# Performance work log

Hardware: AMD Instinct MI355X
Metric: run time of the kernel (lower is better)

The kernel has to match this reference:

```python
import jax, jax.numpy as jnp
import numpy as np

N_NODES = 50000
N_EDGES = 600000
N_GRAPHS = 500
HID = 128
N_LAYERS = 3
N_CLASSES = 10


def setup_inputs() -> dict:
    key = jax.random.key(0)
    ks = jax.random.split(key, 10)
    x = jax.random.normal(ks[0], (N_NODES, HID), dtype=jnp.float32)
    edge_attr = jax.random.normal(ks[1], (N_EDGES, 4), dtype=jnp.float32)
    edge_index = jax.random.randint(ks[2], (2, N_EDGES), 0, N_NODES, dtype=jnp.int32)
    batch = jnp.sort(jax.random.randint(ks[3], (N_NODES,), 0, N_GRAPHS, dtype=jnp.int32))
    s = 1.0 / np.sqrt(HID)
    Wl = jax.random.normal(ks[4], (N_LAYERS, HID, HID), dtype=jnp.float32) * s
    bl = jax.random.normal(ks[5], (N_LAYERS, HID), dtype=jnp.float32) * s
    Wr = jax.random.normal(ks[6], (N_LAYERS, HID, HID), dtype=jnp.float32) * s
    W1 = jax.random.normal(ks[7], (HID, HID), dtype=jnp.float32) * s
    b1 = jnp.zeros((HID,), dtype=jnp.float32)
    W2 = jax.random.normal(ks[8], (N_CLASSES, HID), dtype=jnp.float32) * s
    b2 = jnp.zeros((N_CLASSES,), dtype=jnp.float32)
    return {"x": x, "edge_attr": edge_attr, "edge_index": edge_index, "batch": batch,
            "Wl": Wl, "bl": bl, "Wr": Wr, "W1": W1, "b1": b1, "W2": W2, "b2": b2}


def _sage_conv(x, src, dst, Wl_i, bl_i, Wr_i):
    # mean aggregation of source-node features at target nodes (PyG SAGEConv)
    msg_sum = jax.ops.segment_sum(x[src], dst, num_segments=N_NODES)  # [N, H]
    cnt = jax.ops.segment_sum(jnp.ones((src.shape[0],), x.dtype), dst, num_segments=N_NODES)
    mean = msg_sum / jnp.maximum(cnt, 1.0)[:, None]
    return mean @ Wl_i.T + bl_i + x @ Wr_i.T


def reference(x, edge_attr, edge_index, batch, Wl, bl, Wr, W1, b1, W2, b2):
    # edge_attr is ignored by SAGEConv
    src, dst = edge_index[0], edge_index[1]
    for i in range(N_LAYERS):
        x = jax.nn.relu(_sage_conv(x, src, dst, Wl[i], bl[i], Wr[i]))
    # global_add_pool over graphs
    g = jax.ops.segment_sum(x, batch, num_segments=N_GRAPHS)  # [G, H]
    g = jax.nn.relu(g)
    # dropout p=0.5 is identity at inference
    h = jax.nn.relu(g @ W1.T + b1)
    logits = h @ W2.T + b2
    return jax.nn.log_softmax(logits, axis=1)
```

## Files before the change

kernel.cpp:

```cpp
#include <hip/hip_runtime.h>
#include <math.h>

#define HID 128
#define NCLS 10
#define MAXDEG 32
#define TROWS 32
#define MSP 136

typedef __attribute__((ext_vector_type(8))) short frag8;
typedef __attribute__((ext_vector_type(8))) unsigned short u16x8;
typedef __attribute__((ext_vector_type(4))) float f32x4;

static __device__ __forceinline__ float relu_f(float v) { return v > 0.f ? v : 0.f; }

static __device__ __forceinline__ unsigned short f2bf(float f) {
    unsigned int u = __float_as_uint(f);
    u += 0x7fffu + ((u >> 16) & 1u);
    return (unsigned short)(u >> 16);
}
static __device__ __forceinline__ float bf2f(unsigned short u) {
    return __uint_as_float(((unsigned int)u) << 16);
}

static __device__ __forceinline__ void conv4(const float* __restrict__ in,
                                             unsigned short* __restrict__ out, int i) {
    float4 v = *(const float4*)&in[i * 4];
    ushort4 o;
    o.x = f2bf(v.x); o.y = f2bf(v.y); o.z = f2bf(v.z); o.w = f2bf(v.w);
    *(ushort4*)&out[i * 4] = o;
}

__global__ __launch_bounds__(256) void prep_kernel(const float* __restrict__ x, unsigned short* __restrict__ xb, int nx4,
                                                   const float* __restrict__ Wl, unsigned short* __restrict__ wlb, int nwl4,
                                                   const float* __restrict__ Wr, unsigned short* __restrict__ wrb, int nwr4,
                                                   int* __restrict__ deg, int ndeg4) {
    int i = blockIdx.x * blockDim.x + threadIdx.x;
    if (i < nx4) { conv4(x, xb, i); return; }
    i -= nx4;
    if (i < nwl4) { conv4(Wl, wlb, i); return; }
    i -= nwl4;
    if (i < nwr4) { conv4(Wr, wrb, i); return; }
    i -= nwr4;
    if (i < ndeg4) *(int4*)&deg[i * 4] = make_int4(0, 0, 0, 0);
}

__global__ void fill_kernel(const int* __restrict__ src, const int* __restrict__ dst,
                            int* __restrict__ deg, unsigned short* __restrict__ col, int nE) {
    int e = blockIdx.x * blockDim.x + threadIdx.x;
    if (e < nE) {
        int d = dst[e];
        int p = atomicAdd(&deg[d], 1);
        if (p < MAXDEG) col[(long)d * MAXDEG + p] = (unsigned short)src[e];
    }
}

__global__ __launch_bounds__(256, 6) void sage_kernel(const unsigned short* __restrict__ Xb,
                                                      const int* __restrict__ deg,
                                                      const unsigned short* __restrict__ col,
                                                      const unsigned short* __restrict__ Wlb,
                                                      const unsigned short* __restrict__ Wrb,
                                                      const float* __restrict__ bl,
                                                      unsigned short* __restrict__ Yb, int nN) {
    __shared__ unsigned short ms[TROWS * MSP];

    const int r0 = blockIdx.x * TROWS;

    {
        const int grp = threadIdx.x >> 4;
        const int l16 = threadIdx.x & 15;
        const long fo = (long)l16 * 8;
        for (int i = 0; i < 2; ++i) {
            const int nl = grp * 2 + i;
            const int n = r0 + nl;
            const int d = (n < nN) ? min(deg[n], MAXDEG) : 0;
            const unsigned short* cp = col + (long)n * MAXDEG;

            float acc[8] = {0, 0, 0, 0, 0, 0, 0, 0};

            int p = 0;
            for (; p + 8 <= d; p += 8) {
                int s0 = cp[p],     s1 = cp[p + 1], s2 = cp[p + 2], s3 = cp[p + 3];
                int s4 = cp[p + 4], s5 = cp[p + 5], s6 = cp[p + 6], s7 = cp[p + 7];
                u16x8 v0 = *(const u16x8*)&Xb[(long)s0 * HID + fo];
                u16x8 v1 = *(const u16x8*)&Xb[(long)s1 * HID + fo];
                u16x8 v2 = *(const u16x8*)&Xb[(long)s2 * HID + fo];
                u16x8 v3 = *(const u16x8*)&Xb[(long)s3 * HID + fo];
                u16x8 v4 = *(const u16x8*)&Xb[(long)s4 * HID + fo];
                u16x8 v5 = *(const u16x8*)&Xb[(long)s5 * HID + fo];
                u16x8 v6 = *(const u16x8*)&Xb[(long)s6 * HID + fo];
                u16x8 v7 = *(const u16x8*)&Xb[(long)s7 * HID + fo];
#pragma unroll
                for (int j = 0; j < 8; ++j)
                    acc[j] += ((bf2f(v0[j]) + bf2f(v1[j])) + (bf2f(v2[j]) + bf2f(v3[j]))) +
                              ((bf2f(v4[j]) + bf2f(v5[j])) + (bf2f(v6[j]) + bf2f(v7[j])));
            }
            if (p + 4 <= d) {
                int s0 = cp[p], s1 = cp[p + 1], s2 = cp[p + 2], s3 = cp[p + 3];
                u16x8 v0 = *(const u16x8*)&Xb[(long)s0 * HID + fo];
                u16x8 v1 = *(const u16x8*)&Xb[(long)s1 * HID + fo];
                u16x8 v2 = *(const u16x8*)&Xb[(long)s2 * HID + fo];
                u16x8 v3 = *(const u16x8*)&Xb[(long)s3 * HID + fo];
#pragma unroll
                for (int j = 0; j < 8; ++j)
                    acc[j] += (bf2f(v0[j]) + bf2f(v1[j])) + (bf2f(v2[j]) + bf2f(v3[j]));
                p += 4;
            }
            if (p < d) {
                int s0 = cp[p];
                int s1 = cp[min(p + 1, MAXDEG - 1)];
                int s2 = cp[min(p + 2, MAXDEG - 1)];
                int s3 = cp[min(p + 3, MAXDEG - 1)];
                u16x8 v0 = *(const u16x8*)&Xb[(long)s0 * HID + fo];
                u16x8 v1 = *(const u16x8*)&Xb[(long)s1 * HID + fo];
                u16x8 v2 = *(const u16x8*)&Xb[(long)s2 * HID + fo];
                u16x8 v3 = *(const u16x8*)&Xb[(long)s3 * HID + fo];
#pragma unroll
                for (int j = 0; j < 8; ++j) acc[j] += bf2f(v0[j]);
                if (p + 1 < d) {
#pragma unroll
                    for (int j = 0; j < 8; ++j) acc[j] += bf2f(v1[j]);
                }
                if (p + 2 < d) {
#pragma unroll
                    for (int j = 0; j < 8; ++j) acc[j] += bf2f(v2[j]);
                }
                if (p + 3 < d) {
#pragma unroll
                    for (int j = 0; j < 8; ++j) acc[j] += bf2f(v3[j]);
                }
            }

            const float inv = 1.f / fmaxf((float)d, 1.f);
            u16x8 o;
#pragma unroll
            for (int j = 0; j < 8; ++j) o[j] = f2bf(acc[j] * inv);
            *(u16x8*)&ms[nl * MSP + l16 * 8] = o;
        }
    }
    __syncthreads();

    const int lane = threadIdx.x & 63;
    const int wave = threadIdx.x >> 6;
    const int l15 = lane & 15;
    const int quad = lane >> 4;
    const int wr = wave & 1;
    const int wc = wave >> 1;

    f32x4 acc[4];
#pragma unroll
    for (int ct = 0; ct < 4; ++ct) acc[ct] = (f32x4){0.f, 0.f, 0.f, 0.f};

#pragma unroll
    for (int ks = 0; ks < HID; ks += 32) {
        const int lrow = wr * 16 + l15;
        frag8 aM = *(const frag8*)&ms[lrow * MSP + ks + quad * 8];
        frag8 aX = *(const frag8*)&Xb[(long)(r0 + lrow) * HID + ks + quad * 8];
#pragma unroll
        for (int ct = 0; ct < 4; ++ct) {
            const long nrow = wc * 64 + ct * 16 + l15;
            frag8 bL = *(const frag8*)&Wlb[nrow * HID + ks + quad * 8];
            frag8 bR = *(const frag8*)&Wrb[nrow * HID + ks + quad * 8];
            acc[ct] = __builtin_amdgcn_mfma_f32_16x16x32_bf16(aM, bL, acc[ct], 0, 0, 0);
            acc[ct] = __builtin_amdgcn_mfma_f32_16x16x32_bf16(aX, bR, acc[ct], 0, 0, 0);
        }
    }

#pragma unroll
    for (int ct = 0; ct < 4; ++ct) {
        const int gc = wc * 64 + ct * 16 + l15;
        const float bb = bl[gc];
#pragma unroll
        for (int reg = 0; reg < 4; ++reg) {
            const int gm = r0 + wr * 16 + quad * 4 + reg;
            if (gm < nN) {
                const float v = relu_f(acc[ct][reg] + bb);
                Yb[(long)gm * HID + gc] = f2bf(v);
            }
        }
    }
}

__global__ __launch_bounds__(128) void poolmlp_kernel(const unsigned short* __restrict__ xb,
                                                      const int* __restrict__ batch, int nN,
                                                      const float* __restrict__ W1,
                                                      const float* __restrict__ b1,
                                                      const float* __restrict__ W2,
                                                      const float* __restrict__ b2,
                                                      float* __restrict__ out) {
    __shared__ float gs[HID];
    __shared__ float hs[HID];
    __shared__ float ls[NCLS];
    __shared__ float red[2];
    int gid = blockIdx.x;
    int j = threadIdx.x;

    int lo = 0, hi = nN;
    while (lo < hi) { int mid = (lo + hi) >> 1; if (batch[mid] < gid) lo = mid + 1; else hi = mid; }
    int s = lo;
    hi = nN;
    while (lo < hi) { int mid = (lo + hi) >> 1; if (batch[mid] < gid + 1) lo = mid + 1; else hi = mid; }
    int e = lo;

    float a0 = 0.f, a1 = 0.f, a2 = 0.f, a3 = 0.f;
    int n = s;
    for (; n + 4 <= e; n += 4) {
        a0 += bf2f(xb[(long)n * HID + j]);
        a1 += bf2f(xb[(long)(n + 1) * HID + j]);
        a2 += bf2f(xb[(long)(n + 2) * HID + j]);
        a3 += bf2f(xb[(long)(n + 3) * HID + j]);
    }
    for (; n < e; ++n) a0 += bf2f(xb[(long)n * HID + j]);
    gs[j] = relu_f((a0 + a1) + (a2 + a3));
    __syncthreads();

    float acc = b1[j];
#pragma unroll 8
    for (int k = 0; k < HID; ++k) acc += gs[k] * W1[j * HID + k];
    hs[j] = relu_f(acc);
    __syncthreads();
    if (j < NCLS) {
        float lg = b2[j];
#pragma unroll 8
        for (int k = 0; k < HID; ++k) lg += hs[k] * W2[j * HID + k];
        ls[j] = lg;
    }
    __syncthreads();
    if (j == 0) {
        float m = ls[0];
        for (int c = 1; c < NCLS; ++c) m = fmaxf(m, ls[c]);
        float sum = 0.f;
        for (int c = 0; c < NCLS; ++c) sum += expf(ls[c] - m);
        red[0] = m;
        red[1] = logf(sum);
    }
    __syncthreads();
    if (j < NCLS) out[gid * NCLS + j] = ls[j] - red[0] - red[1];
}


extern "C" void kernel_launch(void* const* d_in, const int* in_sizes, int n_in,
                              void* d_out, int out_size, void* d_ws, size_t ws_size,
                              hipStream_t stream) {
    const float* x_in  = (const float*)d_in[0];
    const int*   eidx  = (const int*)d_in[2];
    const int*   batch = (const int*)d_in[3];
    const float* Wl    = (const float*)d_in[4];
    const float* bl    = (const float*)d_in[5];
    const float* Wr    = (const float*)d_in[6];
    const float* W1    = (const float*)d_in[7];
    const float* b1    = (const float*)d_in[8];
    const float* W2    = (const float*)d_in[9];
    const float* b2    = (const float*)d_in[10];
    float* out = (float*)d_out;

    const int nN = in_sizes[0] / HID;
    const int nE = in_sizes[2] / 2;
    const int nG = out_size / NCLS;
    const int nWl = in_sizes[4];
    const int nWr = in_sizes[6];
    const int nNp = (nN + TROWS - 1) & ~(TROWS - 1);
    const int nTiles = nNp / TROWS;

    const int* src = eidx;
    const int* dst = eidx + nE;

    char* p = (char*)d_ws;
    auto carve = [&](size_t bytes) {
        char* r = p;
        p += (bytes + 255) & ~(size_t)255;
        return r;
    };
    unsigned short* xb  = (unsigned short*)carve((size_t)nNp * HID * 2);
    unsigned short* yb0 = (unsigned short*)carve((size_t)nNp * HID * 2);
    unsigned short* yb1 = (unsigned short*)carve((size_t)nNp * HID * 2);
    unsigned short* wlb = (unsigned short*)carve((size_t)nWl * 2);
    unsigned short* wrb = (unsigned short*)carve((size_t)nWr * 2);
    int*   deg = (int*)carve((size_t)nN * 4);
    unsigned short* col = (unsigned short*)carve((size_t)nN * MAXDEG * 2);
    (void)ws_size; (void)n_in;

    const int nx4 = nN * HID / 4, nwl4 = nWl / 4, nwr4 = nWr / 4, ndeg4 = (nN + 3) / 4;
    const int prep_total = nx4 + nwl4 + nwr4 + ndeg4;
    prep_kernel<<<(prep_total + 255) / 256, 256, 0, stream>>>(
        x_in, xb, nx4, Wl, wlb, nwl4, Wr, wrb, nwr4, deg, ndeg4);

    fill_kernel<<<(nE + 255) / 256, 256, 0, stream>>>(src, dst, deg, col, nE);

    const unsigned short* xcur = xb;
    unsigned short* bufs[2] = {yb0, yb1};
    for (int l = 0; l < 3; ++l) {
        sage_kernel<<<nTiles, 256, 0, stream>>>(
            xcur, deg, col,
            wlb + (size_t)l * HID * HID, wrb + (size_t)l * HID * HID,
            bl + (size_t)l * HID, bufs[l & 1], nN);
        xcur = bufs[l & 1];
    }

    poolmlp_kernel<<<nG, 128, 0, stream>>>(xcur, batch, nN, W1, b1, W2, b2, out);
}
```

Baseline: 316.3 us.

## Stage neighbor gathers via direct global-to-LDS loads with zero-row padding

Replaces the per-thread register gather of neighbor features with global_load_lds (direct global-to-LDS DMA) into per-wave staging buffers, issuing 8 loads per chunk and consuming them with staggered vmcnt waits. Column lists are prefilled with a dummy index pointing at zeroed padding rows, so unused slots gather zeros and tail branches disappear. Neighbor indices are broadcast with shuffles. This adds 32 KB of LDS per block and lowers the launch-bounds occupancy hint from 6 to 3. It also loads full chunks of 8 even for low-degree nodes, which wastes bandwidth, and inline waitcnt asm is fragile.

```diff
diff --git a/kernel.cpp b/kernel.cpp
--- a/kernel.cpp
+++ b/kernel.cpp
@@ -20,6 +20,12 @@
 }
 static __device__ __forceinline__ float bf2f(unsigned short u) {
     return __uint_as_float(((unsigned int)u) << 16);
+}
+
+static __device__ __forceinline__ void gld_lds16(const void* g, void* l) {
+    __builtin_amdgcn_global_load_lds((const __attribute__((address_space(1))) unsigned int*)g,
+                                     (__attribute__((address_space(3))) unsigned int*)l,
+                                     16, 0, 0);
 }
 
 static __device__ __forceinline__ void conv4(const float* __restrict__ in,
@@ -33,7 +39,10 @@
 __global__ __launch_bounds__(256) void prep_kernel(const float* __restrict__ x, unsigned short* __restrict__ xb, int nx4,
                                                    const float* __restrict__ Wl, unsigned short* __restrict__ wlb, int nwl4,
                                                    const float* __restrict__ Wr, unsigned short* __restrict__ wrb, int nwr4,
-                                                   int* __restrict__ deg, int ndeg4) {
+                                                   int* __restrict__ deg, int ndeg4,
+                                                   uint4* __restrict__ colp, int ncol8, unsigned int zpat,
+                                                   uint4* __restrict__ zp0, uint4* __restrict__ zp1,
+                                                   uint4* __restrict__ zp2, int nz8) {
     int i = blockIdx.x * blockDim.x + threadIdx.x;
     if (i < nx4) { conv4(x, xb, i); return; }
     i -= nx4;
@@ -41,7 +50,15 @@
     i -= nwl4;
     if (i < nwr4) { conv4(Wr, wrb, i); return; }
     i -= nwr4;
-    if (i < ndeg4) *(int4*)&deg[i * 4] = make_int4(0, 0, 0, 0);
+    if (i < ndeg4) { *(int4*)&deg[i * 4] = make_int4(0, 0, 0, 0); return; }
+    i -= ndeg4;
+    if (i < ncol8) { colp[i] = make_uint4(zpat, zpat, zpat, zpat); return; }
+    i -= ncol8;
+    if (i < nz8) { zp0[i] = make_uint4(0, 0, 0, 0); return; }
+    i -= nz8;
+    if (i < nz8) { zp1[i] = make_uint4(0, 0, 0, 0); return; }
+    i -= nz8;
+    if (i < nz8) zp2[i] = make_uint4(0, 0, 0, 0);
 }
 
 __global__ void fill_kernel(const int* __restrict__ src, const int* __restrict__ dst,
@@ -54,7 +71,7 @@
     }
 }
 
-__global__ __launch_bounds__(256, 6) void sage_kernel(const unsigned short* __restrict__ Xb,
+__global__ __launch_bounds__(256, 3) void sage_kernel(const unsigned short* __restrict__ Xb,
                                                       const int* __restrict__ deg,
                                                       const unsigned short* __restrict__ col,
                                                       const unsigned short* __restrict__ Wlb,
@@ -62,85 +79,56 @@
                                                       const float* __restrict__ bl,
                                                       unsigned short* __restrict__ Yb, int nN) {
     __shared__ unsigned short ms[TROWS * MSP];
+    __shared__ unsigned short stg[4 * 4096];
 
     const int r0 = blockIdx.x * TROWS;
-
-    {
-        const int grp = threadIdx.x >> 4;
-        const int l16 = threadIdx.x & 15;
-        const long fo = (long)l16 * 8;
-        for (int i = 0; i < 2; ++i) {
-            const int nl = grp * 2 + i;
-            const int n = r0 + nl;
-            const int d = (n < nN) ? min(deg[n], MAXDEG) : 0;
-            const unsigned short* cp = col + (long)n * MAXDEG;
-
-            float acc[8] = {0, 0, 0, 0, 0, 0, 0, 0};
-
-            int p = 0;
-            for (; p + 8 <= d; p += 8) {
-                int s0 = cp[p],     s1 = cp[p + 1], s2 = cp[p + 2], s3 = cp[p + 3];
-                int s4 = cp[p + 4], s5 = cp[p + 5], s6 = cp[p + 6], s7 = cp[p + 7];
-                u16x8 v0 = *(const u16x8*)&Xb[(long)s0 * HID + fo];
-                u16x8 v1 = *(const u16x8*)&Xb[(long)s1 * HID + fo];
-                u16x8 v2 = *(const u16x8*)&Xb[(long)s2 * HID + fo];
-                u16x8 v3 = *(const u16x8*)&Xb[(long)s3 * HID + fo];
-                u16x8 v4 = *(const u16x8*)&Xb[(long)s4 * HID + fo];
-                u16x8 v5 = *(const u16x8*)&Xb[(long)s5 * HID + fo];
-                u16x8 v6 = *(const u16x8*)&Xb[(long)s6 * HID + fo];
-                u16x8 v7 = *(const u16x8*)&Xb[(long)s7 * HID + fo];
-#pragma unroll
-                for (int j = 0; j < 8; ++j)
-                    acc[j] += ((bf2f(v0[j]) + bf2f(v1[j])) + (bf2f(v2[j]) + bf2f(v3[j]))) +
-                              ((bf2f(v4[j]) + bf2f(v5[j])) + (bf2f(v6[j]) + bf2f(v7[j])));
-            }
-            if (p + 4 <= d) {
-                int s0 = cp[p], s1 = cp[p + 1], s2 = cp[p + 2], s3 = cp[p + 3];
-                u16x8 v0 = *(const u16x8*)&Xb[(long)s0 * HID + fo];
-                u16x8 v1 = *(const u16x8*)&Xb[(long)s1 * HID + fo];
-                u16x8 v2 = *(const u16x8*)&Xb[(long)s2 * HID + fo];
-                u16x8 v3 = *(const u16x8*)&Xb[(long)s3 * HID + fo];
-#pragma unroll
-                for (int j = 0; j < 8; ++j)
-                    acc[j] += (bf2f(v0[j]) + bf2f(v1[j])) + (bf2f(v2[j]) + bf2f(v3[j]));
-                p += 4;
-            }
-            if (p < d) {
-                int s0 = cp[p];
-                int s1 = cp[min(p + 1, MAXDEG - 1)];
-                int s2 = cp[min(p + 2, MAXDEG - 1)];
-                int s3 = cp[min(p + 3, MAXDEG - 1)];
-                u16x8 v0 = *(const u16x8*)&Xb[(long)s0 * HID + fo];
-                u16x8 v1 = *(const u16x8*)&Xb[(long)s1 * HID + fo];
-                u16x8 v2 = *(const u16x8*)&Xb[(long)s2 * HID + fo];
-                u16x8 v3 = *(const u16x8*)&Xb[(long)s3 * HID + fo];
-#pragma unroll
-                for (int j = 0; j < 8; ++j) acc[j] += bf2f(v0[j]);
-                if (p + 1 < d) {
-#pragma unroll
-                    for (int j = 0; j < 8; ++j) acc[j] += bf2f(v1[j]);
+    const int lane = threadIdx.x & 63;
+    const int wave = threadIdx.x >> 6;
+    const int grp4 = lane >> 4;
+    const int l16 = lane & 15;
+    const int fo = l16 * 8;
+    unsigned short* stg_w = &stg[wave * 4096];
+
+#pragma unroll
+    for (int set = 0; set < 2; ++set) {
+        const int nl = wave * 8 + set * 4 + grp4;
+        const int n = r0 + nl;
+        const int d = min(deg[n], MAXDEG);
+        const unsigned short* cp = col + (long)n * MAXDEG;
+        const int il = cp[l16];
+        const int ih = cp[16 + l16];
+
+        float acc[8] = {0, 0, 0, 0, 0, 0, 0, 0};
+
+#pragma unroll
+        for (int c = 0; c < 4; ++c) {
+            const bool act = (c * 8 < d);
+            if (act) {
+                asm volatile("s_waitcnt lgkmcnt(0)" ::: "memory");
+#pragma unroll
+                for (int k = 0; k < 8; ++k) {
+                    const int slot = c * 8 + k;
+                    const int idx = (slot < 16) ? __shfl(il, slot, 16) : __shfl(ih, slot - 16, 16);
+                    gld_lds16(Xb + (long)idx * HID + fo, stg_w + k * 512);
                 }
-                if (p + 2 < d) {
-#pragma unroll
-                    for (int j = 0; j < 8; ++j) acc[j] += bf2f(v2[j]);
-                }
-                if (p + 3 < d) {
-#pragma unroll
-                    for (int j = 0; j < 8; ++j) acc[j] += bf2f(v3[j]);
+#pragma unroll
+                for (int k = 0; k < 8; ++k) {
+                    asm volatile("s_waitcnt vmcnt(%0)" ::"i"(7 - k) : "memory");
+                    u16x8 v = *(const u16x8*)&stg_w[k * 512 + lane * 8];
+#pragma unroll
+                    for (int j = 0; j < 8; ++j) acc[j] += bf2f(v[j]);
                 }
             }
-
-            const float inv = 1.f / fmaxf((float)d, 1.f);
-            u16x8 o;
-#pragma unroll
-            for (int j = 0; j < 8; ++j) o[j] = f2bf(acc[j] * inv);
-            *(u16x8*)&ms[nl * MSP + l16 * 8] = o;
         }
-    }
-    __syncthreads();
-
-    const int lane = threadIdx.x & 63;
-    const int wave = threadIdx.x >> 6;
+
+        const float inv = 1.f / fmaxf((float)d, 1.f);
+        u16x8 o;
+#pragma unroll
+        for (int j = 0; j < 8; ++j) o[j] = f2bf(acc[j] * inv);
+        *(u16x8*)&ms[nl * MSP + fo] = o;
+    }
+    __syncthreads();
+
     const int l15 = lane & 15;
     const int quad = lane >> 4;
     const int wr = wave & 1;
@@ -260,6 +248,7 @@
     const int nWr = in_sizes[6];
     const int nNp = (nN + TROWS - 1) & ~(TROWS - 1);
     const int nTiles = nNp / TROWS;
+    const int nRows = nNp + 8;
 
     const int* src = eidx;
     const int* dst = eidx + nE;
@@ -270,19 +259,27 @@
         p += (bytes + 255) & ~(size_t)255;
         return r;
     };
-    unsigned short* xb  = (unsigned short*)carve((size_t)nNp * HID * 2);
-    unsigned short* yb0 = (unsigned short*)carve((size_t)nNp * HID * 2);
-    unsigned short* yb1 = (unsigned short*)carve((size_t)nNp * HID * 2);
+    unsigned short* xb  = (unsigned short*)carve((size_t)nRows * HID * 2);
+    unsigned short* yb0 = (unsigned short*)carve((size_t)nRows * HID * 2);
+    unsigned short* yb1 = (unsigned short*)carve((size_t)nRows * HID * 2);
     unsigned short* wlb = (unsigned short*)carve((size_t)nWl * 2);
     unsigned short* wrb = (unsigned short*)carve((size_t)nWr * 2);
-    int*   deg = (int*)carve((size_t)nN * 4);
-    unsigned short* col = (unsigned short*)carve((size_t)nN * MAXDEG * 2);
+    int*   deg = (int*)carve((size_t)nNp * 4);
+    unsigned short* col = (unsigned short*)carve((size_t)nNp * MAXDEG * 2);
     (void)ws_size; (void)n_in;
 
-    const int nx4 = nN * HID / 4, nwl4 = nWl / 4, nwr4 = nWr / 4, ndeg4 = (nN + 3) / 4;
-    const int prep_total = nx4 + nwl4 + nwr4 + ndeg4;
+    const int nx4 = nN * HID / 4, nwl4 = nWl / 4, nwr4 = nWr / 4;
+    const int ndeg4 = (nNp + 3) / 4;
+    const int ncol8 = nNp * MAXDEG / 8;
+    const int nzrows = nNp + 1 - nN;
+    const int nz8 = nzrows * HID / 8;
+    const unsigned int zpat = (unsigned int)nNp | ((unsigned int)nNp << 16);
+    const int prep_total = nx4 + nwl4 + nwr4 + ndeg4 + ncol8 + 3 * nz8;
     prep_kernel<<<(prep_total + 255) / 256, 256, 0, stream>>>(
-        x_in, xb, nx4, Wl, wlb, nwl4, Wr, wrb, nwr4, deg, ndeg4);
+        x_in, xb, nx4, Wl, wlb, nwl4, Wr, wrb, nwr4, deg, ndeg4,
+        (uint4*)col, ncol8, zpat,
+        (uint4*)(xb + (size_t)nN * HID), (uint4*)(yb0 + (size_t)nN * HID),
+        (uint4*)(yb1 + (size_t)nN * HID), nz8);
 
     fill_kernel<<<(nE + 255) / 256, 256, 0, stream>>>(src, dst, deg, col, nE);
 
```

Measured after the change: 321.0 us. No clear change (+1.5%).
